# Performance work log

Hardware: AMD Instinct MI355X
Metric: run time of the kernel (lower is better)

Reference implementation:

```python
import jax, jax.numpy as jnp
import numpy as np

EPS = 1e-5
RES = [12000, 9000, 6000, 4000]
CH = [9, 64, 128, 256]
SKIPS = 3
FC_N = 128


def batchnorm(x, g, b):
    # train-mode BatchNorm2d over (batch, face) dims; x: [B, C, F]
    m = x.mean(axis=(0, 2), keepdims=True)
    v = x.var(axis=(0, 2), keepdims=True)
    xn = (x - m) * jax.lax.rsqrt(v + EPS)
    return xn * g[None, :, None] + b[None, :, None]


def mesh_conv(x, nbr, w):
    # x: [B, C, F]; nbr: [F, 3] neighbor face ids; w: [O, C, 4]
    n = x[:, :, nbr]                      # [B, C, F, 3] irregular gather
    n1, n2, n3 = n[..., 0], n[..., 1], n[..., 2]
    G = jnp.stack([
        x,
        n1 + n2 + n3,
        jnp.abs(n1 - n2) + jnp.abs(n2 - n3) + jnp.abs(n3 - n1),
        jnp.maximum(jnp.maximum(n1, n2), n3),
    ], axis=-1)                           # [B, C, F, 4] symmetric features
    return jnp.einsum('ocj,bcfj->bof', w, G)


def mres_conv(x, nbr, wc, ws, bng, bnb):
    # MResConvFace: conv0 -> skips x (bn(relu) -> conv) -> +skip -> relu
    x = mesh_conv(x, nbr, wc)
    x1 = x
    for i in range(SKIPS):
        x = batchnorm(jax.nn.relu(x), bng[i], bnb[i])
        x = mesh_conv(x, nbr, ws[i])
    return jax.nn.relu(x + x1)


def setup_inputs() -> dict:
    key = jax.random.key(0)
    ks = jax.random.split(key, 64)
    it = iter(range(64))
    d = {}
    d['x'] = jax.random.normal(ks[next(it)], (8, CH[0], RES[0]), dtype=jnp.float32)
    for i in range(3):
        d[f'nbr{i}'] = jax.random.randint(ks[next(it)], (RES[i], 3), 0, RES[i], dtype=jnp.int32)
        d[f'pool{i}'] = jax.random.randint(ks[next(it)], (RES[i + 1], 3), 0, RES[i], dtype=jnp.int32)
    for i in range(3):
        cin, cout = CH[i], CH[i + 1]
        d[f'wc{i}'] = jax.random.normal(ks[next(it)], (cout, cin, 4), dtype=jnp.float32) * (1.0 / np.sqrt(4 * cin))
        d[f'ws{i}'] = jax.random.normal(ks[next(it)], (SKIPS, cout, cout, 4), dtype=jnp.float32) * (1.0 / np.sqrt(4 * cout))
        d[f'bng{i}'] = jnp.ones((SKIPS, cout), dtype=jnp.float32)
        d[f'bnb{i}'] = jnp.zeros((SKIPS, cout), dtype=jnp.float32)
        d[f'ng{i}'] = jnp.ones((cout,), dtype=jnp.float32)
        d[f'nb{i}'] = jnp.zeros((cout,), dtype=jnp.float32)
    d['fc1_w'] = jax.random.normal(ks[next(it)], (FC_N, CH[-1]), dtype=jnp.float32) * (1.0 / np.sqrt(CH[-1]))
    d['fc1_b'] = jnp.zeros((FC_N,), dtype=jnp.float32)
    d['fc2_w'] = jax.random.normal(ks[next(it)], (1, FC_N), dtype=jnp.float32) * (1.0 / np.sqrt(FC_N))
    d['fc2_b'] = jnp.zeros((1,), dtype=jnp.float32)
    return d


def reference(x, nbr0, nbr1, nbr2, pool0, pool1, pool2,
              wc0, ws0, bng0, bnb0, ng0, nb0,
              wc1, ws1, bng1, bnb1, ng1, nb1,
              wc2, ws2, bng2, bnb2, ng2, nb2,
              fc1_w, fc1_b, fc2_w, fc2_b):
    nbrs = [nbr0, nbr1, nbr2]
    pools = [pool0, pool1, pool2]
    wcs, wss = [wc0, wc1, wc2], [ws0, ws1, ws2]
    bngs, bnbs = [bng0, bng1, bng2], [bnb0, bnb1, bnb2]
    ngs, nbs = [ng0, ng1, ng2], [nb0, nb1, nb2]
    for i in range(3):
        x = mres_conv(x, nbrs[i], wcs[i], wss[i], bngs[i], bnbs[i])
        x = jax.nn.relu(batchnorm(x, ngs[i], nbs[i]))
        x = x[:, :, pools[i]].mean(axis=-1)   # MeshPoolFace: collapse 3 faces -> 1
    x = x.mean(axis=-1)                        # global AvgPool1d over faces -> [B, C]
    h = jax.nn.relu(x @ fc1_w.T + fc1_b)
    return jax.nn.sigmoid(h @ fc2_w.T + fc2_b)  # [B, 1]
```

## Files before the change

kernel.cpp:

```cpp
#include <hip/hip_runtime.h>
#include <math.h>

#define NPART 64
#define TILE_F 16

typedef unsigned short u16;
typedef __attribute__((ext_vector_type(8))) short short8;
typedef __attribute__((ext_vector_type(4))) float f32x4;

__device__ __forceinline__ float relu_(float v){ return fmaxf(v, 0.f); }

__device__ __forceinline__ u16 f2bf(float x){
  unsigned u = __float_as_uint(x);
  u = (u + 0x7fffu + ((u >> 16) & 1u)) >> 16;
  return (u16)u;
}

static __device__ __forceinline__ f32x4 mfma_bf16(short8 a, short8 b, f32x4 c){
  asm("v_mfma_f32_16x16x32_bf16 %0, %1, %2, %0" : "+v"(c) : "v"(a), "v"(b));
  return c;
}

template<int CIN,int COUT,int WR,int NWR,bool BN,bool STATS>
__global__ __launch_bounds__(NWR*(COUT/64)*64) void mconv_kernel(
    const float* __restrict__ xin, const int* __restrict__ nbr,
    const u16* __restrict__ wbf,
    const float* __restrict__ ps_in, const float* __restrict__ gamma,
    const float* __restrict__ beta,
    float* __restrict__ out, float* __restrict__ psum,
    int F, float invN)
{
  constexpr int nWc = COUT/64;
  constexpr int T   = NWR*nWc*64;
  constexpr int BR  = NWR*WR;
  constexpr int K   = 4*CIN;
  constexpr int NSTEP = CIN/16;
  constexpr int ITEMS = (BR*4)/T;
  constexpr int NRF   = WR/16;

  __shared__ __align__(16) u16 Gs[2][BR*64];
  __shared__ float ls[STATS?COUT:1], lq[STATS?COUT:1];
  __shared__ float aS[BN?CIN:1], dS[BN?CIN:1];

  const int t=threadIdx.x, lane=t&63, wid=t>>6;
  const int wm=wid/nWc, wc=wid%nWc;
  const int l15=lane&15, kq=lane>>4;

  if (BN){
    for (int c=t;c<CIN;c+=T){
      float s=0.f,q=0.f;
      #pragma unroll 4
      for (int p=0;p<NPART;p++){ s+=ps_in[p*256+c]; q+=ps_in[(NPART+p)*256+c]; }
      float m=s*invN, v=q*invN-m*m;
      float ai=gamma[c]*rsqrtf(v+1e-5f);
      aS[c]=ai; dS[c]=beta[c]-m*ai;
    }
  }
  if (STATS){ for (int i=t;i<COUT;i+=T){ ls[i]=0.f; lq[i]=0.f; } }
  __syncthreads();

  const float *P0[ITEMS],*P1[ITEMS],*P2[ITEMS],*P3[ITEMS];
  #pragma unroll
  for (int i=0;i<ITEMS;i++){
    int idx=i*T+t, gr=idx>>2, c4q=idx&3;
    int rg=blockIdx.x*BR+gr;
    int b=rg/F, f=rg-b*F;
    int i1=nbr[f*3+0], i2=nbr[f*3+1], i3=nbr[f*3+2];
    const float* xb=xin+(size_t)b*F*CIN+c4q*4;
    P0[i]=xb+(size_t)f *CIN; P1[i]=xb+(size_t)i1*CIN;
    P2[i]=xb+(size_t)i2*CIN; P3[i]=xb+(size_t)i3*CIN;
  }

  const u16* wp = wbf + (size_t)(wc*64+l15)*K + kq*8;
  auto BLD=[&](int cg,int j)->short8{
    return *(const short8*)(wp + (size_t)cg*16*K + (size_t)j*32);
  };
  auto ADS=[&](int pb,int rr,int h)->short8{
    int r=wm*WR+rr*16+l15;
    int sl=h*4+kq;
    return *(const short8*)&Gs[pb][(size_t)r*64 + (size_t)((sl^(r&7))*8)];
  };
  auto GLD=[&](int s,float4 (&g)[ITEMS][4]){
    #pragma unroll
    for (int i=0;i<ITEMS;i++){
      g[i][0]=*(const float4*)(P0[i]+s*16);
      g[i][1]=*(const float4*)(P1[i]+s*16);
      g[i][2]=*(const float4*)(P2[i]+s*16);
      g[i][3]=*(const float4*)(P3[i]+s*16);
    }
  };
  auto BLDW=[&](int pb,int s,float4 (&g)[ITEMS][4]){
    #pragma unroll
    for (int i=0;i<ITEMS;i++){
      int idx=i*T+t, gr=idx>>2, c4q=idx&3;
      float4 S=g[i][0],N1=g[i][1],N2=g[i][2],N3=g[i][3];
      if (BN){
        float4 a4=*(const float4*)&aS[s*16+c4q*4];
        float4 d4=*(const float4*)&dS[s*16+c4q*4];
        S.x =fmaf(relu_(S.x ),a4.x,d4.x); S.y =fmaf(relu_(S.y ),a4.y,d4.y);
        S.z =fmaf(relu_(S.z ),a4.z,d4.z); S.w =fmaf(relu_(S.w ),a4.w,d4.w);
        N1.x=fmaf(relu_(N1.x),a4.x,d4.x); N1.y=fmaf(relu_(N1.y),a4.y,d4.y);
        N1.z=fmaf(relu_(N1.z),a4.z,d4.z); N1.w=fmaf(relu_(N1.w),a4.w,d4.w);
        N2.x=fmaf(relu_(N2.x),a4.x,d4.x); N2.y=fmaf(relu_(N2.y),a4.y,d4.y);
        N2.z=fmaf(relu_(N2.z),a4.z,d4.z); N2.w=fmaf(relu_(N2.w),a4.w,d4.w);
        N3.x=fmaf(relu_(N3.x),a4.x,d4.x); N3.y=fmaf(relu_(N3.y),a4.y,d4.y);
        N3.z=fmaf(relu_(N3.z),a4.z,d4.z); N3.w=fmaf(relu_(N3.w),a4.w,d4.w);
      }
      short8 lo,hi;
      #define FEAT(dst,i0,sv,av,bv,cv) \
        dst[i0+0]=(short)f2bf(sv); \
        dst[i0+1]=(short)f2bf(av+bv+cv); \
        dst[i0+2]=(short)f2bf(fabsf(av-bv)+fabsf(bv-cv)+fabsf(cv-av)); \
        dst[i0+3]=(short)f2bf(fmaxf(fmaxf(av,bv),cv));
      FEAT(lo,0,S.x,N1.x,N2.x,N3.x)
      FEAT(lo,4,S.y,N1.y,N2.y,N3.y)
      FEAT(hi,0,S.z,N1.z,N2.z,N3.z)
      FEAT(hi,4,S.w,N1.w,N2.w,N3.w)
      #undef FEAT
      u16* rowp=&Gs[pb][(size_t)gr*64];
      *(short8*)&rowp[(size_t)(((2*c4q  )^(gr&7))*8)]=lo;
      *(short8*)&rowp[(size_t)(((2*c4q+1)^(gr&7))*8)]=hi;
    }
  };

  f32x4 acc[NRF][4];
  #pragma unroll
  for (int rr=0;rr<NRF;rr++)
    #pragma unroll
    for (int cg=0;cg<4;cg++){ f32x4 z={0.f,0.f,0.f,0.f}; acc[rr][cg]=z; }

  short8 B0[4],B1[4];
  #pragma unroll
  for (int cg=0;cg<4;cg++) B0[cg]=BLD(cg,0);
  #pragma unroll
  for (int cg=0;cg<4;cg++) B1[cg]=BLD(cg,1);

  { float4 g0[ITEMS][4]; GLD(0,g0); BLDW(0,0,g0); }
  __syncthreads();

  #pragma unroll 2
  for (int s=0;s<NSTEP;s++){
    const int pb=s&1;
    float4 g[ITEMS][4];
    if (s+1<NSTEP) GLD(s+1,g);
    short8 A[NRF];
    #pragma unroll
    for (int rr=0;rr<NRF;rr++) A[rr]=ADS(pb,rr,0);
    #pragma unroll
    for (int rr=0;rr<NRF;rr++)
      #pragma unroll
      for (int cg=0;cg<4;cg++) acc[rr][cg]=mfma_bf16(A[rr],B0[cg],acc[rr][cg]);
    if (s+1<NSTEP){
      #pragma unroll
      for (int cg=0;cg<4;cg++) B0[cg]=BLD(cg,2*(s+1));
    }
    #pragma unroll
    for (int rr=0;rr<NRF;rr++) A[rr]=ADS(pb,rr,1);
    #pragma unroll
    for (int rr=0;rr<NRF;rr++)
      #pragma unroll
      for (int cg=0;cg<4;cg++) acc[rr][cg]=mfma_bf16(A[rr],B1[cg],acc[rr][cg]);
    if (s+1<NSTEP){
      #pragma unroll
      for (int cg=0;cg<4;cg++) B1[cg]=BLD(cg,2*(s+1)+1);
      BLDW(pb^1,s+1,g);
    }
    __syncthreads();
  }

  #pragma unroll
  for (int cg=0;cg<4;cg++){
    const int col=wc*64+cg*16+l15;
    float rs=0.f,rq=0.f;
    #pragma unroll
    for (int rr=0;rr<NRF;rr++){
      const size_t rbase=(size_t)blockIdx.x*BR + wm*WR + rr*16 + kq*4;
      #pragma unroll
      for (int q=0;q<4;q++){
        float v=acc[rr][cg][q];
        out[(rbase+q)*COUT+col]=v;
        if (STATS){ float rv=relu_(v); rs+=rv; rq+=rv*rv; }
      }
    }
    if (STATS){ atomicAdd(&ls[col],rs); atomicAdd(&lq[col],rq); }
  }
  if (STATS){
    __syncthreads();
    const int part=blockIdx.x&(NPART-1);
    for (int i=t;i<COUT;i+=T){
      atomicAdd(&psum[(size_t)part*256+i],ls[i]);
      atomicAdd(&psum[(size_t)(NPART+part)*256+i],lq[i]);
    }
  }
}

template<int CIN,int COUT,bool BN,bool STATS>
__global__ __launch_bounds__(256) void conv_kernel(
    const float* __restrict__ xin, const int* __restrict__ nbr,
    const float* __restrict__ Wt, const float* __restrict__ bn_a,
    const float* __restrict__ bn_d,
    float* __restrict__ out, float* __restrict__ psum, int F)
{
  constexpr int K = 4*CIN;
  constexpr int ROWLEN = K + 4;
  __shared__ float Gs[TILE_F][ROWLEN];
  __shared__ int   nI[TILE_F*3];
  __shared__ float ls[STATS?COUT:1];
  __shared__ float lq[STATS?COUT:1];
  const int t = threadIdx.x;
  const int fbase = blockIdx.x*TILE_F;
  const int b = blockIdx.y;
  const float* __restrict__ xb = xin + (size_t)b*F*CIN;

  if (t < TILE_F*3){ int fi=t/3, j=t-fi*3; int fg=fbase+fi; nI[t]=(fg<F)?nbr[fg*3+j]:0; }
  if (STATS){ for (int i=t;i<COUT;i+=256){ ls[i]=0.f; lq[i]=0.f; } }
  __syncthreads();

  for (int idx=t; idx<TILE_F*CIN; idx+=256){
    int fi=idx/CIN, c=idx-fi*CIN;
    int fg=fbase+fi;
    float* dst=&Gs[fi][4*c];
    if (fg<F){
      int i1=nI[fi*3], i2=nI[fi*3+1], i3=nI[fi*3+2];
      float s =xb[(size_t)fg*CIN+c];
      float v1=xb[(size_t)i1*CIN+c];
      float v2=xb[(size_t)i2*CIN+c];
      float v3=xb[(size_t)i3*CIN+c];
      if (BN){ float a=bn_a[c], dd=bn_d[c];
        s=fmaf(relu_(s),a,dd); v1=fmaf(relu_(v1),a,dd);
        v2=fmaf(relu_(v2),a,dd); v3=fmaf(relu_(v3),a,dd); }
      dst[0]=s; dst[1]=v1+v2+v3;
      dst[2]=fabsf(v1-v2)+fabsf(v2-v3)+fabsf(v3-v1);
      dst[3]=fmaxf(fmaxf(v1,v2),v3);
    } else { dst[0]=0.f;dst[1]=0.f;dst[2]=0.f;dst[3]=0.f; }
  }
  __syncthreads();

  constexpr int OQ=COUT/4;
  constexpr int R=256/OQ;
  constexpr int FPT=TILE_F/R;
  const int col=t%OQ, row=t/OQ;
  const int o0=col*4, f0=row*FPT;
  float4 acc[FPT];
  #pragma unroll
  for (int fi=0;fi<FPT;fi++){ acc[fi].x=0.f;acc[fi].y=0.f;acc[fi].z=0.f;acc[fi].w=0.f; }

  for (int k=0;k<K;k+=4){
    float4 w0=*(const float4*)&Wt[(size_t)(k+0)*COUT+o0];
    float4 w1=*(const float4*)&Wt[(size_t)(k+1)*COUT+o0];
    float4 w2=*(const float4*)&Wt[(size_t)(k+2)*COUT+o0];
    float4 w3=*(const float4*)&Wt[(size_t)(k+3)*COUT+o0];
    #pragma unroll
    for (int fi=0;fi<FPT;fi++){
      float4 g=*(const float4*)&Gs[f0+fi][k];
      acc[fi].x=fmaf(g.x,w0.x,fmaf(g.y,w1.x,fmaf(g.z,w2.x,fmaf(g.w,w3.x,acc[fi].x))));
      acc[fi].y=fmaf(g.x,w0.y,fmaf(g.y,w1.y,fmaf(g.z,w2.y,fmaf(g.w,w3.y,acc[fi].y))));
      acc[fi].z=fmaf(g.x,w0.z,fmaf(g.y,w1.z,fmaf(g.z,w2.z,fmaf(g.w,w3.z,acc[fi].z))));
      acc[fi].w=fmaf(g.x,w0.w,fmaf(g.y,w1.w,fmaf(g.z,w2.w,fmaf(g.w,w3.w,acc[fi].w))));
    }
  }

  float4 rs={0,0,0,0}, rq={0,0,0,0};
  #pragma unroll
  for (int fi=0;fi<FPT;fi++){
    int fg=fbase+f0+fi;
    if (fg<F){
      *(float4*)&out[((size_t)b*F+fg)*COUT+o0]=acc[fi];
      if (STATS){
        float rx=relu_(acc[fi].x), ry=relu_(acc[fi].y);
        float rz=relu_(acc[fi].z), rw=relu_(acc[fi].w);
        rs.x+=rx; rs.y+=ry; rs.z+=rz; rs.w+=rw;
        rq.x+=rx*rx; rq.y+=ry*ry; rq.z+=rz*rz; rq.w+=rw*rw;
      }
    }
  }
  if (STATS){
    atomicAdd(&ls[o0+0],rs.x); atomicAdd(&ls[o0+1],rs.y);
    atomicAdd(&ls[o0+2],rs.z); atomicAdd(&ls[o0+3],rs.w);
    atomicAdd(&lq[o0+0],rq.x); atomicAdd(&lq[o0+1],rq.y);
    atomicAdd(&lq[o0+2],rq.z); atomicAdd(&lq[o0+3],rq.w);
    __syncthreads();
    int part=(blockIdx.y*gridDim.x+blockIdx.x)&(NPART-1);
    for (int i=t;i<COUT;i+=256){
      atomicAdd(&psum[(size_t)part*256+i], ls[i]);
      atomicAdd(&psum[(size_t)(NPART+part)*256+i], lq[i]);
    }
  }
}

template<int C>
__global__ __launch_bounds__(256) void add_relu_stats_kernel(
    const float* __restrict__ y0, float* __restrict__ z,
    float* __restrict__ psum, int n4)
{
  __shared__ float ls[C], lq[C];
  for (int i=threadIdx.x;i<C;i+=256){ ls[i]=0.f; lq[i]=0.f; }
  __syncthreads();
  int i0=blockIdx.x*256+threadIdx.x;
  int stride=gridDim.x*256;
  int c0=(i0*4)%C;
  float4 rs={0,0,0,0}, rq={0,0,0,0};
  for (int i=i0;i<n4;i+=stride){
    float4 a=*(const float4*)&y0[(size_t)i*4];
    float4 bq=*(const float4*)&z[(size_t)i*4];
    float4 v;
    v.x=relu_(a.x+bq.x); v.y=relu_(a.y+bq.y);
    v.z=relu_(a.z+bq.z); v.w=relu_(a.w+bq.w);
    *(float4*)&z[(size_t)i*4]=v;
    rs.x+=v.x; rs.y+=v.y; rs.z+=v.z; rs.w+=v.w;
    rq.x+=v.x*v.x; rq.y+=v.y*v.y; rq.z+=v.z*v.z; rq.w+=v.w*v.w;
  }
  atomicAdd(&ls[c0+0],rs.x); atomicAdd(&ls[c0+1],rs.y);
  atomicAdd(&ls[c0+2],rs.z); atomicAdd(&ls[c0+3],rs.w);
  atomicAdd(&lq[c0+0],rq.x); atomicAdd(&lq[c0+1],rq.y);
  atomicAdd(&lq[c0+2],rq.z); atomicAdd(&lq[c0+3],rq.w);
  __syncthreads();
  int part=blockIdx.x&(NPART-1);
  for (int i=threadIdx.x;i<C;i+=256){
    atomicAdd(&psum[(size_t)part*256+i],ls[i]);
    atomicAdd(&psum[(size_t)(NPART+part)*256+i],lq[i]);
  }
}

__global__ __launch_bounds__(256) void pool_kernel(
    const float* __restrict__ z, const int* __restrict__ pl,
    const float* __restrict__ ps_in, const float* __restrict__ gamma,
    const float* __restrict__ beta,
    float* __restrict__ out, int C4, int F, int Fn, int n4, float invN)
{
  __shared__ float aS[256], dS[256];
  const int C=C4*4;
  const int t=threadIdx.x;
  if (t<C){
    float s=0.f,q=0.f;
    #pragma unroll 4
    for (int p=0;p<NPART;p++){ s+=ps_in[p*256+t]; q+=ps_in[(NPART+p)*256+t]; }
    float m=s*invN, v=q*invN-m*m;
    float ai=gamma[t]*rsqrtf(v+1e-5f);
    aS[t]=ai; dS[t]=beta[t]-m*ai;
  }
  __syncthreads();
  for (int i=blockIdx.x*256+t; i<n4; i+=gridDim.x*256){
    int c4=i%C4; int rest=i/C4; int p=rest%Fn; int b=rest/Fn;
    int p0=pl[p*3], p1=pl[p*3+1], p2=pl[p*3+2];
    float4 a4=*(const float4*)&aS[4*c4], d4=*(const float4*)&dS[4*c4];
    float4 v0=*(const float4*)&z[((size_t)b*F+p0)*C+4*c4];
    float4 v1=*(const float4*)&z[((size_t)b*F+p1)*C+4*c4];
    float4 v2=*(const float4*)&z[((size_t)b*F+p2)*C+4*c4];
    float4 r;
    r.x=(relu_(fmaf(v0.x,a4.x,d4.x))+relu_(fmaf(v1.x,a4.x,d4.x))+relu_(fmaf(v2.x,a4.x,d4.x)))*(1.f/3.f);
    r.y=(relu_(fmaf(v0.y,a4.y,d4.y))+relu_(fmaf(v1.y,a4.y,d4.y))+relu_(fmaf(v2.y,a4.y,d4.y)))*(1.f/3.f);
    r.z=(relu_(fmaf(v0.z,a4.z,d4.z))+relu_(fmaf(v1.z,a4.z,d4.z))+relu_(fmaf(v2.z,a4.z,d4.z)))*(1.f/3.f);
    r.w=(relu_(fmaf(v0.w,a4.w,d4.w))+relu_(fmaf(v1.w,a4.w,d4.w))+relu_(fmaf(v2.w,a4.w,d4.w)))*(1.f/3.f);
    *(float4*)&out[((size_t)b*Fn+p)*C+4*c4]=r;
  }
}

__global__ __launch_bounds__(256) void colsum_kernel(
    const float* __restrict__ x, float* __restrict__ bc, int F, int chunk)
{
  int b=blockIdx.y; int f0=blockIdx.x*chunk;
  int c=threadIdx.x;
  int fe=f0+chunk; if (fe>F) fe=F;
  float s=0.f;
  for (int f=f0;f<fe;f++) s+=x[((size_t)b*F+f)*256+c];
  atomicAdd(&bc[b*256+c], s);
}

__global__ __launch_bounds__(256) void head_kernel(
    const float* __restrict__ bc, const float* __restrict__ w1,
    const float* __restrict__ b1, const float* __restrict__ w2,
    const float* __restrict__ b2, float* __restrict__ outp, float invF)
{
  __shared__ float xm[8*256];
  __shared__ float h[8*128];
  int t=threadIdx.x;
  for (int i=t;i<2048;i+=256) xm[i]=bc[i]*invF;
  __syncthreads();
  #pragma unroll
  for (int r=0;r<4;r++){
    int idx=t+r*256; int b=idx>>7, j=idx&127;
    float s=b1[j];
    for (int c=0;c<256;c++) s=fmaf(xm[b*256+c],w1[j*256+c],s);
    h[idx]=relu_(s);
  }
  __syncthreads();
  if (t<8){
    float s=b2[0];
    for (int j=0;j<128;j++) s=fmaf(h[t*128+j],w2[j],s);
    outp[t]=1.f/(1.f+expf(-s));
  }
}

__global__ __launch_bounds__(256) void transpose_in_kernel(
    const float* __restrict__ x, float* __restrict__ xt, int F)
{
  int i=blockIdx.x*256+threadIdx.x;
  int total=8*9*F;
  if (i<total){ int f=i%F; int c=(i/F)%9; int b=i/(9*F);
    xt[((size_t)b*F+f)*9+c]=x[i]; }
}

__global__ __launch_bounds__(256) void transpose_w_kernel(
    const float* __restrict__ w, float* __restrict__ wt, int K, int COUT)
{
  int i=blockIdx.x*256+threadIdx.x;
  if (i<K*COUT){ int o=i/K, k=i-o*K; wt[(size_t)k*COUT+o]=w[i]; }
}

__global__ __launch_bounds__(256) void cvt_bf16_kernel(
    const float* __restrict__ w, u16* __restrict__ o, int n)
{
  int i=blockIdx.x*256+threadIdx.x;
  if (i<n) o[i]=f2bf(w[i]);
}


template<int CIN,int COUT,int WR,int NWR,bool BN,bool STATS>
static void launch_mconv(const float* xin, const int* nbr, const u16* wbf,
                         const float* ps_in, const float* gamma, const float* beta,
                         float* out, float* ps_out, int F, float invN,
                         hipStream_t stream)
{
  constexpr int T  = NWR*(COUT/64)*64;
  constexpr int BR = NWR*WR;
  int M = 8*F;
  mconv_kernel<CIN,COUT,WR,NWR,BN,STATS><<<M/BR, T, 0, stream>>>(
      xin,nbr,wbf,ps_in,gamma,beta,out,ps_out,F,invN);
}

extern "C" void kernel_launch(void* const* d_in, const int* in_sizes, int n_in,
                              void* d_out, int out_size, void* d_ws, size_t ws_size,
                              hipStream_t stream)
{
  const float* x    =(const float*)d_in[0];
  const int*  nbr0  =(const int*)d_in[1];
  const int*  pool0 =(const int*)d_in[2];
  const int*  nbr1  =(const int*)d_in[3];
  const int*  pool1 =(const int*)d_in[4];
  const int*  nbr2  =(const int*)d_in[5];
  const int*  pool2 =(const int*)d_in[6];
  const float* wc0  =(const float*)d_in[7];
  const float* ws0  =(const float*)d_in[8];
  const float* bng0 =(const float*)d_in[9];
  const float* bnb0 =(const float*)d_in[10];
  const float* ng0  =(const float*)d_in[11];
  const float* nb0  =(const float*)d_in[12];
  const float* wc1  =(const float*)d_in[13];
  const float* ws1  =(const float*)d_in[14];
  const float* bng1 =(const float*)d_in[15];
  const float* bnb1 =(const float*)d_in[16];
  const float* ng1  =(const float*)d_in[17];
  const float* nb1  =(const float*)d_in[18];
  const float* wc2  =(const float*)d_in[19];
  const float* ws2  =(const float*)d_in[20];
  const float* bng2 =(const float*)d_in[21];
  const float* bnb2 =(const float*)d_in[22];
  const float* ng2  =(const float*)d_in[23];
  const float* nb2  =(const float*)d_in[24];
  const float* fc1w =(const float*)d_in[25];
  const float* fc1b =(const float*)d_in[26];
  const float* fc2w =(const float*)d_in[27];
  const float* fc2b =(const float*)d_in[28];
  float* outp=(float*)d_out;

  char* base=(char*)d_ws;
  size_t off=0;
  auto alloc=[&](size_t nbytes)->void*{
    void* p=base+off; off=(off+nbytes+255)&~(size_t)255; return p; };

  float* psum0 =(float*)alloc((size_t)12*131072);
  float* bc    =(float*)alloc(8192);
  float* wt_wc0=(float*)alloc((size_t)36*64*4);
  u16*   bws0  =(u16*)alloc((size_t)3*16384*2);
  u16*   bwc1  =(u16*)alloc((size_t)32768*2);
  u16*   bws1  =(u16*)alloc((size_t)3*65536*2);
  u16*   bwc2  =(u16*)alloc((size_t)131072*2);
  u16*   bws2  =(u16*)alloc((size_t)3*262144*2);
  float* xT    =(float*)alloc((size_t)8*12000*9*4);
  float* B0    =(float*)alloc((size_t)49152000);
  float* B1    =(float*)alloc((size_t)49152000);
  float* B2    =(float*)alloc((size_t)49152000);
  if (off>ws_size) return;

  auto PS=[&](int i){ return psum0+(size_t)i*32768; };

  hipMemsetAsync(psum0,0,(size_t)12*131072+8192,stream);

  { int n=8*9*12000; transpose_in_kernel<<<(n+255)/256,256,0,stream>>>(x,xT,12000); }
  { int n=36*64; transpose_w_kernel<<<(n+255)/256,256,0,stream>>>(wc0,wt_wc0,36,64); }
  auto cv=[&](const float* w,u16* o,int n){
    cvt_bf16_kernel<<<(n+255)/256,256,0,stream>>>(w,o,n); };
  cv(ws0,bws0,3*16384);
  cv(wc1,bwc1,32768);
  cv(ws1,bws1,3*65536);
  cv(wc2,bwc2,131072);
  cv(ws2,bws2,3*262144);

  {
    const int F=12000; const float invN=1.f/(8.f*F);
    dim3 grid((F+TILE_F-1)/TILE_F, 8);
    conv_kernel<9,64,false,true><<<grid,256,0,stream>>>(xT,nbr0,wt_wc0,nullptr,nullptr,B0,PS(0),F);
    launch_mconv<64,64,32,2,true,true >(B0,nbr0,bws0,        PS(0),bng0,     bnb0,     B1,PS(1),F,invN,stream);
    launch_mconv<64,64,32,2,true,true >(B1,nbr0,bws0+16384,  PS(1),bng0+64,  bnb0+64,  B2,PS(2),F,invN,stream);
    launch_mconv<64,64,32,2,true,false>(B2,nbr0,bws0+32768,  PS(2),bng0+128, bnb0+128, B1,nullptr,F,invN,stream);
    int n4=8*F*64/4;
    int g=(n4+255)/256; if (g>2048) g=2048;
    add_relu_stats_kernel<64><<<g,256,0,stream>>>(B0,B1,PS(3),n4);
    int n4p=8*9000*16; int gp=(n4p+255)/256; if (gp>2048) gp=2048;
    pool_kernel<<<gp,256,0,stream>>>(B1,pool0,PS(3),ng0,nb0,B2,16,F,9000,n4p,invN);
  }
  {
    const int F=9000; const float invN=1.f/(8.f*F);
    launch_mconv<64,128,64,1,false,true >(B2,nbr1,bwc1,         nullptr,nullptr,  nullptr,  B0,PS(4),F,invN,stream);
    launch_mconv<128,128,64,1,true,true >(B0,nbr1,bws1,         PS(4),bng1,      bnb1,     B1,PS(5),F,invN,stream);
    launch_mconv<128,128,64,1,true,true >(B1,nbr1,bws1+65536,   PS(5),bng1+128,  bnb1+128, B2,PS(6),F,invN,stream);
    launch_mconv<128,128,64,1,true,false>(B2,nbr1,bws1+131072,  PS(6),bng1+256,  bnb1+256, B1,nullptr,F,invN,stream);
    int n4=8*F*128/4;
    int g=(n4+255)/256; if (g>2048) g=2048;
    add_relu_stats_kernel<128><<<g,256,0,stream>>>(B0,B1,PS(7),n4);
    int n4p=8*6000*32; int gp=(n4p+255)/256; if (gp>2048) gp=2048;
    pool_kernel<<<gp,256,0,stream>>>(B1,pool1,PS(7),ng1,nb1,B0,32,F,6000,n4p,invN);
  }
  {
    const int F=6000; const float invN=1.f/(8.f*F);
    launch_mconv<128,256,64,1,false,true >(B0,nbr2,bwc2,         nullptr,nullptr,  nullptr,  B1,PS(8),F,invN,stream);
    launch_mconv<256,256,64,1,true,true >(B1,nbr2,bws2,         PS(8), bng2,     bnb2,     B2,PS(9),F,invN,stream);
    launch_mconv<256,256,64,1,true,true >(B2,nbr2,bws2+262144,  PS(9), bng2+256, bnb2+256, B0,PS(10),F,invN,stream);
    launch_mconv<256,256,64,1,true,false>(B0,nbr2,bws2+524288,  PS(10),bng2+512, bnb2+512, B2,nullptr,F,invN,stream);
    int n4=8*F*256/4;
    int g=(n4+255)/256; if (g>2048) g=2048;
    add_relu_stats_kernel<256><<<g,256,0,stream>>>(B1,B2,PS(11),n4);
    int n4p=8*4000*64; int gp=(n4p+255)/256; if (gp>2048) gp=2048;
    pool_kernel<<<gp,256,0,stream>>>(B2,pool2,PS(11),ng2,nb2,B0,64,F,4000,n4p,invN);
    colsum_kernel<<<dim3(16,8),256,0,stream>>>(B0,bc,4000,250);
  }
  head_kernel<<<1,256,0,stream>>>(bc,fc1w,fc1b,fc2w,fc2b,outp,1.f/4000.f);
}
```

Baseline: 982.9 us.

## Fuse residual add-relu-stats into last skip conv and deepen gather prefetch

Removes the separate add_relu_stats kernel by having the final skip mesh-conv of each stage add the residual, apply relu, write output and accumulate BN statistics in its epilogue. This saves a full read-modify-write pass over the activation tensor and three launches. It also restructures the K loop into a two-stage-ahead gather prefetch using two register buffers, which adds register pressure and could lower occupancy.

New measurement: 965.9 us. Within noise of the previous version (-1.7%).

```diff
diff --git a/kernel.cpp b/kernel.cpp
--- a/kernel.cpp
+++ b/kernel.cpp
@@ -21,12 +21,12 @@
   return c;
 }
 
-template<int CIN,int COUT,int WR,int NWR,bool BN,bool STATS>
+template<int CIN,int COUT,int WR,int NWR,bool BN,bool STATS,bool RES>
 __global__ __launch_bounds__(NWR*(COUT/64)*64) void mconv_kernel(
     const float* __restrict__ xin, const int* __restrict__ nbr,
     const u16* __restrict__ wbf,
     const float* __restrict__ ps_in, const float* __restrict__ gamma,
-    const float* __restrict__ beta,
+    const float* __restrict__ beta, const float* __restrict__ res,
     float* __restrict__ out, float* __restrict__ psum,
     int F, float invN)
 {
@@ -135,14 +135,7 @@
   #pragma unroll
   for (int cg=0;cg<4;cg++) B1[cg]=BLD(cg,1);
 
-  { float4 g0[ITEMS][4]; GLD(0,g0); BLDW(0,0,g0); }
-  __syncthreads();
-
-  #pragma unroll 2
-  for (int s=0;s<NSTEP;s++){
-    const int pb=s&1;
-    float4 g[ITEMS][4];
-    if (s+1<NSTEP) GLD(s+1,g);
+  auto MSTEP=[&](int pb,int s){
     short8 A[NRF];
     #pragma unroll
     for (int rr=0;rr<NRF;rr++) A[rr]=ADS(pb,rr,0);
@@ -163,8 +156,22 @@
     if (s+1<NSTEP){
       #pragma unroll
       for (int cg=0;cg<4;cg++) B1[cg]=BLD(cg,2*(s+1)+1);
-      BLDW(pb^1,s+1,g);
-    }
+    }
+  };
+
+  float4 gA[ITEMS][4], gB[ITEMS][4];
+  GLD(0,gA); BLDW(0,0,gA);
+  GLD(1,gA);
+  __syncthreads();
+
+  for (int s=0;s<NSTEP;s+=2){
+    if (s+2<NSTEP) GLD(s+2,gB);
+    MSTEP(0,s);
+    if (s+1<NSTEP) BLDW(1,s+1,gA);
+    __syncthreads();
+    if (s+3<NSTEP) GLD(s+3,gA);
+    if (s+1<NSTEP) MSTEP(1,s+1);
+    if (s+2<NSTEP) BLDW(0,s+2,gB);
     __syncthreads();
   }
 
@@ -177,9 +184,11 @@
       const size_t rbase=(size_t)blockIdx.x*BR + wm*WR + rr*16 + kq*4;
       #pragma unroll
       for (int q=0;q<4;q++){
+        size_t idx=(rbase+q)*COUT+col;
         float v=acc[rr][cg][q];
-        out[(rbase+q)*COUT+col]=v;
-        if (STATS){ float rv=relu_(v); rs+=rv; rq+=rv*rv; }
+        if (RES){ v += res[idx]; v = relu_(v); }
+        out[idx]=v;
+        if (STATS){ float rv = RES ? v : relu_(v); rs+=rv; rq+=rv*rv; }
       }
     }
     if (STATS){ atomicAdd(&ls[col],rs); atomicAdd(&lq[col],rq); }
@@ -288,40 +297,6 @@
   }
 }
 
-template<int C>
-__global__ __launch_bounds__(256) void add_relu_stats_kernel(
-    const float* __restrict__ y0, float* __restrict__ z,
-    float* __restrict__ psum, int n4)
-{
-  __shared__ float ls[C], lq[C];
-  for (int i=threadIdx.x;i<C;i+=256){ ls[i]=0.f; lq[i]=0.f; }
-  __syncthreads();
-  int i0=blockIdx.x*256+threadIdx.x;
-  int stride=gridDim.x*256;
-  int c0=(i0*4)%C;
-  float4 rs={0,0,0,0}, rq={0,0,0,0};
-  for (int i=i0;i<n4;i+=stride){
-    float4 a=*(const float4*)&y0[(size_t)i*4];
-    float4 bq=*(const float4*)&z[(size_t)i*4];
-    float4 v;
-    v.x=relu_(a.x+bq.x); v.y=relu_(a.y+bq.y);
-    v.z=relu_(a.z+bq.z); v.w=relu_(a.w+bq.w);
-    *(float4*)&z[(size_t)i*4]=v;
-    rs.x+=v.x; rs.y+=v.y; rs.z+=v.z; rs.w+=v.w;
-    rq.x+=v.x*v.x; rq.y+=v.y*v.y; rq.z+=v.z*v.z; rq.w+=v.w*v.w;
-  }
-  atomicAdd(&ls[c0+0],rs.x); atomicAdd(&ls[c0+1],rs.y);
-  atomicAdd(&ls[c0+2],rs.z); atomicAdd(&ls[c0+3],rs.w);
-  atomicAdd(&lq[c0+0],rq.x); atomicAdd(&lq[c0+1],rq.y);
-  atomicAdd(&lq[c0+2],rq.z); atomicAdd(&lq[c0+3],rq.w);
-  __syncthreads();
-  int part=blockIdx.x&(NPART-1);
-  for (int i=threadIdx.x;i<C;i+=256){
-    atomicAdd(&psum[(size_t)part*256+i],ls[i]);
-    atomicAdd(&psum[(size_t)(NPART+part)*256+i],lq[i]);
-  }
-}
-
 __global__ __launch_bounds__(256) void pool_kernel(
     const float* __restrict__ z, const int* __restrict__ pl,
     const float* __restrict__ ps_in, const float* __restrict__ gamma,
@@ -416,17 +391,17 @@
 }
 
 
-template<int CIN,int COUT,int WR,int NWR,bool BN,bool STATS>
+template<int CIN,int COUT,int WR,int NWR,bool BN,bool STATS,bool RES>
 static void launch_mconv(const float* xin, const int* nbr, const u16* wbf,
                          const float* ps_in, const float* gamma, const float* beta,
-                         float* out, float* ps_out, int F, float invN,
-                         hipStream_t stream)
+                         const float* res, float* out, float* ps_out,
+                         int F, float invN, hipStream_t stream)
 {
   constexpr int T  = NWR*(COUT/64)*64;
   constexpr int BR = NWR*WR;
   int M = 8*F;
-  mconv_kernel<CIN,COUT,WR,NWR,BN,STATS><<<M/BR, T, 0, stream>>>(
-      xin,nbr,wbf,ps_in,gamma,beta,out,ps_out,F,invN);
+  mconv_kernel<CIN,COUT,WR,NWR,BN,STATS,RES><<<M/BR, T, 0, stream>>>(
+      xin,nbr,wbf,ps_in,gamma,beta,res,out,ps_out,F,invN);
 }
 
 extern "C" void kernel_launch(void* const* d_in, const int* in_sizes, int n_in,
@@ -501,36 +476,27 @@
     const int F=12000; const float invN=1.f/(8.f*F);
     dim3 grid((F+TILE_F-1)/TILE_F, 8);
     conv_kernel<9,64,false,true><<<grid,256,0,stream>>>(xT,nbr0,wt_wc0,nullptr,nullptr,B0,PS(0),F);
-    launch_mconv<64,64,32,2,true,true >(B0,nbr0,bws0,        PS(0),bng0,     bnb0,     B1,PS(1),F,invN,stream);
-    launch_mconv<64,64,32,2,true,true >(B1,nbr0,bws0+16384,  PS(1),bng0+64,  bnb0+64,  B2,PS(2),F,invN,stream);
-    launch_mconv<64,64,32,2,true,false>(B2,nbr0,bws0+32768,  PS(2),bng0+128, bnb0+128, B1,nullptr,F,invN,stream);
-    int n4=8*F*64/4;
-    int g=(n4+255)/256; if (g>2048) g=2048;
-    add_relu_stats_kernel<64><<<g,256,0,stream>>>(B0,B1,PS(3),n4);
+    launch_mconv<64,64,32,2,true,true ,false>(B0,nbr0,bws0,        PS(0),bng0,     bnb0,     nullptr,B1,PS(1),F,invN,stream);
+    launch_mconv<64,64,32,2,true,true ,false>(B1,nbr0,bws0+16384,  PS(1),bng0+64,  bnb0+64,  nullptr,B2,PS(2),F,invN,stream);
+    launch_mconv<64,64,32,2,true,true ,true >(B2,nbr0,bws0+32768,  PS(2),bng0+128, bnb0+128, B0,     B1,PS(3),F,invN,stream);
     int n4p=8*9000*16; int gp=(n4p+255)/256; if (gp>2048) gp=2048;
     pool_kernel<<<gp,256,0,stream>>>(B1,pool0,PS(3),ng0,nb0,B2,16,F,9000,n4p,invN);
   }
   {
     const int F=9000; const float invN=1.f/(8.f*F);
-    launch_mconv<64,128,64,1,false,true >(B2,nbr1,bwc1,         nullptr,nullptr,  nullptr,  B0,PS(4),F,invN,stream);
-    launch_mconv<128,128,64,1,true,true >(B0,nbr1,bws1,         PS(4),bng1,      bnb1,     B1,PS(5),F,invN,stream);
-    launch_mconv<128,128,64,1,true,true >(B1,nbr1,bws1+65536,   PS(5),bng1+128,  bnb1+128, B2,PS(6),F,invN,stream);
-    launch_mconv<128,128,64,1,true,false>(B2,nbr1,bws1+131072,  PS(6),bng1+256,  bnb1+256, B1,nullptr,F,invN,stream);
-    int n4=8*F*128/4;
-    int g=(n4+255)/256; if (g>2048) g=2048;
-    add_relu_stats_kernel<128><<<g,256,0,stream>>>(B0,B1,PS(7),n4);
+    launch_mconv<64,128,64,1,false,true ,false>(B2,nbr1,bwc1,         nullptr,nullptr,  nullptr,  nullptr,B0,PS(4),F,invN,stream);
+    launch_mconv<128,128,64,1,true,true ,false>(B0,nbr1,bws1,         PS(4),bng1,      bnb1,     nullptr,B1,PS(5),F,invN,stream);
+    launch_mconv<128,128,64,1,true,true ,false>(B1,nbr1,bws1+65536,   PS(5),bng1+128,  bnb1+128, nullptr,B2,PS(6),F,invN,stream);
+    launch_mconv<128,128,64,1,true,true ,true >(B2,nbr1,bws1+131072,  PS(6),bng1+256,  bnb1+256, B0,     B1,PS(7),F,invN,stream);
     int n4p=8*6000*32; int gp=(n4p+255)/256; if (gp>2048) gp=2048;
     pool_kernel<<<gp,256,0,stream>>>(B1,pool1,PS(7),ng1,nb1,B0,32,F,6000,n4p,invN);
   }
   {
     const int F=6000; const float invN=1.f/(8.f*F);
-    launch_mconv<128,256,64,1,false,true >(B0,nbr2,bwc2,         nullptr,nullptr,  nullptr,  B1,PS(8),F,invN,stream);
-    launch_mconv<256,256,64,1,true,true >(B1,nbr2,bws2,         PS(8), bng2,     bnb2,     B2,PS(9),F,invN,stream);
-    launch_mconv<256,256,64,1,true,true >(B2,nbr2,bws2+262144,  PS(9), bng2+256, bnb2+256, B0,PS(10),F,invN,stream);
-    launch_mconv<256,256,64,1,true,false>(B0,nbr2,bws2+524288,  PS(10),bng2+512, bnb2+512, B2,nullptr,F,invN,stream);
-    int n4=8*F*256/4;
-    int g=(n4+255)/256; if (g>2048) g=2048;
-    add_relu_stats_kernel<256><<<g,256,0,stream>>>(B1,B2,PS(11),n4);
+    launch_mconv<128,256,64,1,false,true ,false>(B0,nbr2,bwc2,         nullptr,nullptr,  nullptr,  nullptr,B1,PS(8),F,invN,stream);
+    launch_mconv<256,256,64,1,true,true ,false>(B1,nbr2,bws2,         PS(8), bng2,     bnb2,     nullptr,B2,PS(9),F,invN,stream);
+    launch_mconv<256,256,64,1,true,true ,false>(B2,nbr2,bws2+262144,  PS(9), bng2+256, bnb2+256, nullptr,B0,PS(10),F,invN,stream);
+    launch_mconv<256,256,64,1,true,true ,true >(B0,nbr2,bws2+524288,  PS(10),bng2+512, bnb2+512, B1,     B2,PS(11),F,invN,stream);
     int n4p=8*4000*64; int gp=(n4p+255)/256; if (gp>2048) gp=2048;
     pool_kernel<<<gp,256,0,stream>>>(B2,pool2,PS(11),ng2,nb2,B0,64,F,4000,n4p,invN);
     colsum_kernel<<<dim3(16,8),256,0,stream>>>(B0,bc,4000,250);
```
